# Optimization experiments

Hardware: AMD Instinct MI355X
Metric: run time of the kernel (lower is better)

Reference implementation:

```python
import jax, jax.numpy as jnp
import numpy as np

NUM_SCOPES, NUM_DECOMPS, BATCH, NODES_IN, NUM_SUMS = 128, 8, 1024, 32, 32


def logmatmul(a, b):
    """Stable log-domain matmul: out[..., b, j] = logsumexp_k(a[..., b, k] + b[..., k, j]).
    a: [s, d, B, K], b: [s, d, K, J] -> [s, d, B, J]."""
    max_a = jnp.max(a, axis=-1, keepdims=True)            # [s, d, B, 1]
    max_b = jnp.max(b, axis=-2, keepdims=True)            # [s, d, 1, J]
    prod = jnp.einsum('sdbk,sdkj->sdbj', jnp.exp(a - max_a), jnp.exp(b - max_b))
    return jnp.log(prod) + max_a + max_b


def setup_inputs() -> dict:
    key = jax.random.key(0)
    k1, k2 = jax.random.split(key)
    x = jax.random.normal(k1, (NUM_SCOPES, NUM_DECOMPS, BATCH, NODES_IN), dtype=jnp.float32)
    # accumulators are linear-space (logspace_accumulators=False) and must be > 0
    accumulators = jax.random.uniform(
        k2, (NUM_SCOPES, NUM_DECOMPS, NODES_IN, NUM_SUMS),
        minval=0.1, maxval=1.0, dtype=jnp.float32)
    return {"x": x, "accumulators": accumulators}


def reference(x, accumulators):
    # log_softmax over the nodes_in axis (axis=2) of log(accumulators)
    log_weights = jax.nn.log_softmax(jnp.log(accumulators), axis=2)
    return logmatmul(x, log_weights)  # [s, d, B, num_sums]
```

## Files before the change

kernel.cpp:

```cpp
#include <hip/hip_runtime.h>
#include <stdint.h>


#define THREADS 256
#define ROWS    128
#define WPITCH  40

typedef __attribute__((ext_vector_type(8))) short short8;
typedef __attribute__((ext_vector_type(4))) float f32x4;
typedef __attribute__((ext_vector_type(4))) int   i32x4;

__device__ __forceinline__ uint32_t pack2_bf16(float lo, float hi) {
    uint32_t ul = __builtin_bit_cast(uint32_t, lo);
    uint32_t uh = __builtin_bit_cast(uint32_t, hi);
    ul = (ul + 0x7fffu + ((ul >> 16) & 1u)) >> 16;
    uh = (uh + 0x7fffu + ((uh >> 16) & 1u)) >> 16;
    return ul | (uh << 16);
}

__device__ __forceinline__ unsigned short bf16_1(float v) {
    uint32_t u = __builtin_bit_cast(uint32_t, v);
    return (unsigned short)((u + 0x7fffu + ((u >> 16) & 1u)) >> 16);
}

__global__ __launch_bounds__(THREADS, 8) void sws_kernel(
    const float* __restrict__ x,
    const float* __restrict__ acc,
    float* __restrict__ out)
{
    __shared__ float w_f32[32 * 32];
    __shared__ float inv_lds[32];
    __shared__ __align__(16) unsigned short wt_lds[32 * WPITCH];

    const int t    = threadIdx.x;
    const int blk  = blockIdx.x;
    const int sd   = blk >> 3;
    const int lane = t & 63;
    const int wv   = t >> 6;
    const int l15  = lane & 15;
    const int quad = lane >> 4;

    const float4* x4 = (const float4*)(x + (size_t)blk * ROWS * 32);
    float4 xv[4];
#pragma unroll
    for (int i = 0; i < 2; ++i) {
        int f4 = ((wv * 2 + i) * 16 + l15) * 8 + quad * 2;
        xv[2 * i]     = x4[f4];
        xv[2 * i + 1] = x4[f4 + 1];
    }

    const float4 a4 = ((const float4*)(acc + (size_t)sd * 1024))[t];
    *((float4*)&w_f32[t * 4]) = a4;
    __syncthreads();
    if (t < 32) {
        float s = 0.f;
#pragma unroll
        for (int k = 0; k < 32; ++k) s += w_f32[k * 32 + t];
        inv_lds[t] = 1.0f / s;
    }
    __syncthreads();
    {
        const int k = t >> 3, j0 = (t & 7) * 4;
        const float4 inv4 = *((const float4*)&inv_lds[j0]);
        wt_lds[(j0 + 0) * WPITCH + k] = bf16_1(a4.x * inv4.x);
        wt_lds[(j0 + 1) * WPITCH + k] = bf16_1(a4.y * inv4.y);
        wt_lds[(j0 + 2) * WPITCH + k] = bf16_1(a4.z * inv4.z);
        wt_lds[(j0 + 3) * WPITCH + k] = bf16_1(a4.w * inv4.w);
    }

    float  mrow[2];
    short8 afrag[2];
#pragma unroll
    for (int i = 0; i < 2; ++i) {
        float4 a = xv[2 * i], b = xv[2 * i + 1];
        float m = fmaxf(fmaxf(fmaxf(a.x, a.y), fmaxf(a.z, a.w)),
                        fmaxf(fmaxf(b.x, b.y), fmaxf(b.z, b.w)));
        m = fmaxf(m, __shfl_xor(m, 16, 64));
        m = fmaxf(m, __shfl_xor(m, 32, 64));
        mrow[i] = m;
        i32x4 pk;
        pk[0] = (int)pack2_bf16(__expf(a.x - m), __expf(a.y - m));
        pk[1] = (int)pack2_bf16(__expf(a.z - m), __expf(a.w - m));
        pk[2] = (int)pack2_bf16(__expf(b.x - m), __expf(b.y - m));
        pk[3] = (int)pack2_bf16(__expf(b.z - m), __expf(b.w - m));
        afrag[i] = __builtin_bit_cast(short8, pk);
    }
    __syncthreads();

    short8 bfrag[2];
#pragma unroll
    for (int jt = 0; jt < 2; ++jt)
        bfrag[jt] = *(const short8*)&wt_lds[(jt * 16 + l15) * WPITCH + quad * 8];

    f32x4 cacc[2][2];
#pragma unroll
    for (int i = 0; i < 2; ++i)
#pragma unroll
        for (int jt = 0; jt < 2; ++jt)
            cacc[i][jt] = __builtin_amdgcn_mfma_f32_16x16x32_bf16(
                bfrag[jt], afrag[i], (f32x4){0.f, 0.f, 0.f, 0.f}, 0, 0, 0);

    float* ob = out + (size_t)blk * ROWS * 32;
#pragma unroll
    for (int i = 0; i < 2; ++i) {
        float* orow = ob + (size_t)((wv * 2 + i) * 16 + l15) * 32;
        const float mr = mrow[i];
#pragma unroll
        for (int jt = 0; jt < 2; ++jt) {
            f32x4 c = cacc[i][jt];
            float4 o;
            o.x = __logf(c[0]) + mr;
            o.y = __logf(c[1]) + mr;
            o.z = __logf(c[2]) + mr;
            o.w = __logf(c[3]) + mr;
            *(float4*)(orow + jt * 16 + quad * 4) = o;
        }
    }
}

extern "C" void kernel_launch(void* const* d_in, const int* in_sizes, int n_in,
                              void* d_out, int out_size, void* d_ws, size_t ws_size,
                              hipStream_t stream) {
    const float* x   = (const float*)d_in[0];
    const float* acc = (const float*)d_in[1];
    float* out = (float*)d_out;

    dim3 grid(8192);
    dim3 block(THREADS);
    hipLaunchKernelGGL(sws_kernel, grid, block, 0, stream, x, acc, out);
}
```

Measured before the change: 228.2 us.

## Build weight fragments in registers via shuffles instead of LDS and barriers

Each wave now loads its own column slices of the accumulator matrix straight into registers. It computes the column sums with in-wave shuffles and packs the normalized bf16 B fragments directly. This removes all shared memory and the three block barriers. Output stores are also made nontemporal. The cost is redundant accumulator loads and normalization in every wave, plus strided scalar global loads of the weights.

After: 239.6 us. 1.05x slower.

```diff
diff --git a/kernel.cpp b/kernel.cpp
--- a/kernel.cpp
+++ b/kernel.cpp
@@ -4,7 +4,6 @@
 
 #define THREADS 256
 #define ROWS    128
-#define WPITCH  40
 
 typedef __attribute__((ext_vector_type(8))) short short8;
 typedef __attribute__((ext_vector_type(4))) float f32x4;
@@ -18,20 +17,11 @@
     return ul | (uh << 16);
 }
 
-__device__ __forceinline__ unsigned short bf16_1(float v) {
-    uint32_t u = __builtin_bit_cast(uint32_t, v);
-    return (unsigned short)((u + 0x7fffu + ((u >> 16) & 1u)) >> 16);
-}
-
 __global__ __launch_bounds__(THREADS, 8) void sws_kernel(
     const float* __restrict__ x,
     const float* __restrict__ acc,
     float* __restrict__ out)
 {
-    __shared__ float w_f32[32 * 32];
-    __shared__ float inv_lds[32];
-    __shared__ __align__(16) unsigned short wt_lds[32 * WPITCH];
-
     const int t    = threadIdx.x;
     const int blk  = blockIdx.x;
     const int sd   = blk >> 3;
@@ -40,8 +30,8 @@
     const int l15  = lane & 15;
     const int quad = lane >> 4;
 
-    const float4* x4 = (const float4*)(x + (size_t)blk * ROWS * 32);
-    float4 xv[4];
+    const f32x4* x4 = (const f32x4*)(x + (size_t)blk * ROWS * 32);
+    f32x4 xv[4];
 #pragma unroll
     for (int i = 0; i < 2; ++i) {
         int f4 = ((wv * 2 + i) * 16 + l15) * 8 + quad * 2;
@@ -49,48 +39,48 @@
         xv[2 * i + 1] = x4[f4 + 1];
     }
 
-    const float4 a4 = ((const float4*)(acc + (size_t)sd * 1024))[t];
-    *((float4*)&w_f32[t * 4]) = a4;
-    __syncthreads();
-    if (t < 32) {
-        float s = 0.f;
+    const float* ab = acc + (size_t)sd * 1024 + (quad * 8) * 32 + l15;
+    float racc0[8], racc1[8];
 #pragma unroll
-        for (int k = 0; k < 32; ++k) s += w_f32[k * 32 + t];
-        inv_lds[t] = 1.0f / s;
-    }
-    __syncthreads();
-    {
-        const int k = t >> 3, j0 = (t & 7) * 4;
-        const float4 inv4 = *((const float4*)&inv_lds[j0]);
-        wt_lds[(j0 + 0) * WPITCH + k] = bf16_1(a4.x * inv4.x);
-        wt_lds[(j0 + 1) * WPITCH + k] = bf16_1(a4.y * inv4.y);
-        wt_lds[(j0 + 2) * WPITCH + k] = bf16_1(a4.z * inv4.z);
-        wt_lds[(j0 + 3) * WPITCH + k] = bf16_1(a4.w * inv4.w);
-    }
+    for (int e = 0; e < 8; ++e) racc0[e] = ab[e * 32];
+#pragma unroll
+    for (int e = 0; e < 8; ++e) racc1[e] = ab[e * 32 + 16];
 
     float  mrow[2];
     short8 afrag[2];
 #pragma unroll
     for (int i = 0; i < 2; ++i) {
-        float4 a = xv[2 * i], b = xv[2 * i + 1];
-        float m = fmaxf(fmaxf(fmaxf(a.x, a.y), fmaxf(a.z, a.w)),
-                        fmaxf(fmaxf(b.x, b.y), fmaxf(b.z, b.w)));
+        f32x4 a = xv[2 * i], b = xv[2 * i + 1];
+        float m = fmaxf(fmaxf(fmaxf(a[0], a[1]), fmaxf(a[2], a[3])),
+                        fmaxf(fmaxf(b[0], b[1]), fmaxf(b[2], b[3])));
         m = fmaxf(m, __shfl_xor(m, 16, 64));
         m = fmaxf(m, __shfl_xor(m, 32, 64));
         mrow[i] = m;
         i32x4 pk;
-        pk[0] = (int)pack2_bf16(__expf(a.x - m), __expf(a.y - m));
-        pk[1] = (int)pack2_bf16(__expf(a.z - m), __expf(a.w - m));
-        pk[2] = (int)pack2_bf16(__expf(b.x - m), __expf(b.y - m));
-        pk[3] = (int)pack2_bf16(__expf(b.z - m), __expf(b.w - m));
+        pk[0] = (int)pack2_bf16(__expf(a[0] - m), __expf(a[1] - m));
+        pk[1] = (int)pack2_bf16(__expf(a[2] - m), __expf(a[3] - m));
+        pk[2] = (int)pack2_bf16(__expf(b[0] - m), __expf(b[1] - m));
+        pk[3] = (int)pack2_bf16(__expf(b[2] - m), __expf(b[3] - m));
         afrag[i] = __builtin_bit_cast(short8, pk);
     }
-    __syncthreads();
 
     short8 bfrag[2];
+    {
+        float s0 = 0.f, s1 = 0.f;
 #pragma unroll
-    for (int jt = 0; jt < 2; ++jt)
-        bfrag[jt] = *(const short8*)&wt_lds[(jt * 16 + l15) * WPITCH + quad * 8];
+        for (int e = 0; e < 8; ++e) { s0 += racc0[e]; s1 += racc1[e]; }
+        s0 += __shfl_xor(s0, 16, 64);  s0 += __shfl_xor(s0, 32, 64);
+        s1 += __shfl_xor(s1, 16, 64);  s1 += __shfl_xor(s1, 32, 64);
+        const float inv0 = 1.0f / s0, inv1 = 1.0f / s1;
+        i32x4 p0, p1;
+#pragma unroll
+        for (int w = 0; w < 4; ++w) {
+            p0[w] = (int)pack2_bf16(racc0[2 * w] * inv0, racc0[2 * w + 1] * inv0);
+            p1[w] = (int)pack2_bf16(racc1[2 * w] * inv1, racc1[2 * w + 1] * inv1);
+        }
+        bfrag[0] = __builtin_bit_cast(short8, p0);
+        bfrag[1] = __builtin_bit_cast(short8, p1);
+    }
 
     f32x4 cacc[2][2];
 #pragma unroll
@@ -108,12 +98,12 @@
 #pragma unroll
         for (int jt = 0; jt < 2; ++jt) {
             f32x4 c = cacc[i][jt];
-            float4 o;
-            o.x = __logf(c[0]) + mr;
-            o.y = __logf(c[1]) + mr;
-            o.z = __logf(c[2]) + mr;
-            o.w = __logf(c[3]) + mr;
-            *(float4*)(orow + jt * 16 + quad * 4) = o;
+            f32x4 o;
+            o[0] = __logf(c[0]) + mr;
+            o[1] = __logf(c[1]) + mr;
+            o[2] = __logf(c[2]) + mr;
+            o[3] = __logf(c[3]) + mr;
+            __builtin_nontemporal_store(o, (f32x4*)(orow + jt * 16 + quad * 4));
         }
     }
 }
```
